# Kernel optimization log

Measured on AMD Instinct MI355X. Metric: run time of the kernel, lower is better.

The kernel has to match this reference:

```python
import jax, jax.numpy as jnp
import numpy as np

# Irrep layout of node_vec: 128x0e | 64x1e (64*3) | 32x2e (32*5)
MUL0, MUL1, MUL2 = 128, 64, 32
A = 32  # node_attr scalar channels (32x0e)
N = 8192


def setup_inputs() -> dict:
    key = jax.random.key(0)
    ks = jax.random.split(key, 12)
    f32 = jnp.float32
    return {
        "node_vec": jax.random.normal(ks[0], (N, MUL0 + 3 * MUL1 + 5 * MUL2), f32),
        "node_embedding": jax.random.normal(ks[1], (N, A), f32),
        # fctp_1: TP(input, attr) -> gated irreps (scalars + gates + vectors)
        "W1s": jax.random.normal(ks[2], (MUL0, A, MUL0), f32),          # 0e x 0e -> 0e
        "b1s": jnp.zeros((MUL0,), f32),
        "W1g": jax.random.normal(ks[3], (MUL0, A, MUL1 + MUL2), f32),   # 0e x 0e -> gate 0e
        "b1g": jnp.zeros((MUL1 + MUL2,), f32),
        "W1v1": jax.random.normal(ks[4], (MUL1, A, MUL1), f32),         # 1e x 0e -> 1e
        "W1v2": jax.random.normal(ks[5], (MUL2, A, MUL2), f32),         # 2e x 0e -> 2e
        # fctp_2: TP(mlp_mid, attr) -> 32x0e (only scalar path allowed by CG rules)
        "W2": jax.random.normal(ks[6], (MUL0, A, A), f32),
        "b2": jnp.zeros((A,), f32),
        # output network: LinearRS(32->32) + SiLU + LinearRS(32->1)
        "W3": jax.random.normal(ks[7], (A, A), f32),
        "b3": jnp.zeros((A,), f32),
        "W4": jax.random.normal(ks[8], (A, 1), f32),
        "b4": jnp.zeros((1,), f32),
    }


def reference(node_vec, node_embedding, W1s, b1s, W1g, b1g, W1v1, W1v2, W2, b2, W3, b3, W4, b4):
    n = node_vec.shape[0]
    attr = node_embedding
    # split features by irrep degree
    s = node_vec[:, :MUL0]                                         # [n,128]   0e
    v1 = node_vec[:, MUL0:MUL0 + 3 * MUL1].reshape(n, MUL1, 3)     # [n,64,3]  1e
    v2 = node_vec[:, MUL0 + 3 * MUL1:].reshape(n, MUL2, 5)         # [n,32,5]  2e

    inv = lambda u: 1.0 / np.sqrt(u * A).astype(np.float32)

    # ---- fctp_1: fully-connected TP with scalar attr (l x 0e -> l per-path mixing) ----
    s_mid = jnp.einsum('nu,nv,uvw->nw', s, attr, W1s) * inv(MUL0) + b1s
    g = jnp.einsum('nu,nv,uvw->nw', s, attr, W1g) * inv(MUL0) + b1g
    v1_mid = jnp.einsum('num,nv,uvw->nwm', v1, attr, W1v1) * inv(MUL1)
    v2_mid = jnp.einsum('num,nv,uvw->nwm', v2, attr, W1v2) * inv(MUL2)

    # ---- SwishGate: SiLU on scalars, sigmoid gates on vectors ----
    s_act = jax.nn.silu(s_mid)
    gate = jax.nn.sigmoid(g)
    v1_g = v1_mid * gate[:, :MUL1, None]
    v2_g = v2_mid * gate[:, MUL1:, None]
    # NOTE: v1_g/v2_g have no allowed CG path into the 0e output of fctp_2 (l x 0 -> 0
    # only for l=0), so they do not contribute — exactly as in the original module.
    del v1_g, v2_g

    # ---- fctp_2: mlp_mid x attr -> 32x0e (scalar path only) ----
    h = jnp.einsum('nu,nv,uvw->nw', s_act, attr, W2) * inv(MUL0) + b2

    # ---- output network: LinearRS + SiLU + LinearRS ----
    h = jax.nn.silu(h @ (W3 / np.sqrt(A).astype(np.float32)) + b3)
    pred_energy = h @ (W4 / np.sqrt(A).astype(np.float32)) + b4     # [n,1]
    return pred_energy
```

## Files before the change

kernel.cpp:

```cpp
#include <hip/hip_runtime.h>

typedef _Float16 f16;
typedef f16 f16x8 __attribute__((ext_vector_type(8)));
typedef f16 f16x4 __attribute__((ext_vector_type(4)));
typedef f16 f16x2 __attribute__((ext_vector_type(2)));
typedef float f32x4 __attribute__((ext_vector_type(4)));

union F8 { uint4 u4; f16x8 v; f16x2 h[4]; f16 e[8]; };

__global__ __launch_bounds__(256) void prep_kernel(
    const float* __restrict__ node_vec, const float* __restrict__ attr,
    const float* __restrict__ W1s, const float* __restrict__ W2,
    f16* __restrict__ s_f16, f16* __restrict__ attr_f16,
    f16* __restrict__ W1P, f16* __restrict__ W2P)
{
    __shared__ f16 T[32 * 36];
    const int b = blockIdx.x, t = threadIdx.x;

    if (b < 640) {
        const float* src; f16* dst; int u, w0, W;
        if (b < 512) { u = b >> 2; w0 = (b & 3) * 32; W = 128; src = W1s; dst = W1P; }
        else         { u = b - 512; w0 = 0;           W = 32;  src = W2;  dst = W2P; }
        {
            int v = t >> 3, wq = t & 7;
            float4 f = *(const float4*)(src + (size_t)(u * 32 + v) * W + w0 + wq * 4);
            T[v * 36 + wq * 4 + 0] = (f16)f.x;
            T[v * 36 + wq * 4 + 1] = (f16)f.y;
            T[v * 36 + wq * 4 + 2] = (f16)f.z;
            T[v * 36 + wq * 4 + 3] = (f16)f.w;
        }
        __syncthreads();
        {
            int w = t >> 3, vr = t & 7;
            f16x4 o = { T[(vr * 4 + 0) * 36 + w], T[(vr * 4 + 1) * 36 + w],
                        T[(vr * 4 + 2) * 36 + w], T[(vr * 4 + 3) * 36 + w] };
            *(f16x4*)(dst + (size_t)u * (W * 32) + (size_t)(w0 + w) * 32 + vr * 4) = o;
        }
    } else if (b < 1152) {
        int j = (b - 640) * 256 + t;
        int n = j >> 4, c = j & 15;
        float4 a  = *(const float4*)(node_vec + (size_t)n * 480 + c * 8);
        float4 bb = *(const float4*)(node_vec + (size_t)n * 480 + c * 8 + 4);
        f16x8 ev = { (f16)a.x, (f16)a.y, (f16)a.z, (f16)a.w,
                     (f16)bb.x, (f16)bb.y, (f16)bb.z, (f16)bb.w };
        *(f16x8*)(s_f16 + (size_t)n * 128 + c * 8) = ev;
    } else {
        int j = (b - 1152) * 256 + t;
        int n = j >> 2, c = j & 3;
        float4 a  = *(const float4*)(attr + (size_t)n * 32 + c * 8);
        float4 bb = *(const float4*)(attr + (size_t)n * 32 + c * 8 + 4);
        f16x8 ev = { (f16)a.x, (f16)a.y, (f16)a.z, (f16)a.w,
                     (f16)bb.x, (f16)bb.y, (f16)bb.z, (f16)bb.w };
        *(f16x8*)(attr_f16 + (size_t)n * 32 + c * 8) = ev;
    }
}

__global__ __launch_bounds__(256, 2) void gemm1_kernel(
    const f16* __restrict__ s_f16, const f16* __restrict__ attr_f16,
    const f16* __restrict__ W1P, const float* __restrict__ b1s,
    f16* __restrict__ s_act)
{
    __shared__ alignas(16) f16 s_lds[64 * 136];

    const int t  = threadIdx.x;
    const int n0 = blockIdx.x * 64;
    const int l  = t & 63, lr = l & 15, q = l >> 4;
    const int c0 = blockIdx.y * 64 + (t >> 6) * 16;

    const f16* Bp = W1P + ((size_t)(c0 + lr)) * 32 + q * 8;
    f16x8 B[8];
    #pragma unroll
    for (int j = 0; j < 8; ++j)
        B[j] = *(const f16x8*)(Bp + (size_t)j * 4096);

    F8 af[4];
    #pragma unroll
    for (int mt = 0; mt < 4; ++mt)
        af[mt].v = *(const f16x8*)(attr_f16 + (size_t)(n0 + 16 * mt + lr) * 32 + q * 8);

    #pragma unroll
    for (int i = 0; i < 4; ++i) {
        int ch = t + 256 * i;
        int r = ch >> 4, c8 = ch & 15;
        *(uint4*)(s_lds + r * 136 + c8 * 8) =
            *(const uint4*)(s_f16 + (size_t)(n0 + r) * 128 + c8 * 8);
    }
    __syncthreads();

    f32x4 acc[4] = { {0,0,0,0}, {0,0,0,0}, {0,0,0,0}, {0,0,0,0} };

    F8 s8[2][4];
    #pragma unroll
    for (int mt = 0; mt < 4; ++mt)
        s8[0][mt].v = *(const f16x8*)(s_lds + (16 * mt + lr) * 136);

    #pragma unroll 4
    for (int uo = 0; uo < 16; ++uo) {
        const int cur = uo & 1, nxt = cur ^ 1;
        const int uon = (uo + 1 < 16) ? uo + 1 : 15;
        #pragma unroll
        for (int mt = 0; mt < 4; ++mt)
            s8[nxt][mt].v = *(const f16x8*)(s_lds + (16 * mt + lr) * 136 + uon * 8);
        #pragma unroll
        for (int j = 0; j < 8; ++j) {
            const int u = uo * 8 + j;
            f16x8 bf = B[j];
            const int un = (u + 8 < 128) ? (u + 8) : u;
            B[j] = *(const f16x8*)(Bp + (size_t)un * 4096);
            #pragma unroll
            for (int mt = 0; mt < 4; ++mt) {
                f16 sv = s8[cur][mt].e[j];
                f16x2 sb = { sv, sv };
                F8 a;
                #pragma unroll
                for (int kk = 0; kk < 4; ++kk)
                    a.h[kk] = sb * af[mt].h[kk];
                acc[mt] = __builtin_amdgcn_mfma_f32_16x16x32_f16(a.v, bf, acc[mt], 0, 0, 0);
            }
        }
    }

    const float bv = b1s[c0 + lr];
    #pragma unroll
    for (int mt = 0; mt < 4; ++mt)
        #pragma unroll
        for (int reg = 0; reg < 4; ++reg) {
            int row = n0 + 16 * mt + q * 4 + reg;
            float v = acc[mt][reg] * 0.015625f + bv;
            s_act[(size_t)row * 128 + c0 + lr] = (f16)(v / (1.f + __expf(-v)));
        }
}

__global__ __launch_bounds__(256, 2) void gemm2_head_kernel(
    const f16* __restrict__ s_act, const f16* __restrict__ attr_f16,
    const f16* __restrict__ W2P, const float* __restrict__ b2,
    const float* __restrict__ W3, const float* __restrict__ b3,
    const float* __restrict__ W4, const float* __restrict__ b4,
    float* __restrict__ out)
{
    __shared__ alignas(16) f16 s_lds[32 * 136];
    __shared__ alignas(16) float red[4][32 * 36];
    __shared__ alignas(16) float W3_lds[32 * 36];
    __shared__ alignas(16) float h_lds[32 * 36];

    const int t  = threadIdx.x;
    const int n0 = blockIdx.x * 32;
    const int wv = t >> 6, l = t & 63, lr = l & 15, q = l >> 4;
    const int u0 = wv * 32;

    const f16* B2p = W2P + ((size_t)u0 * 32 + lr) * 32 + q * 8;
    f16x8 B0[8], B1[8];
    #pragma unroll
    for (int j = 0; j < 8; ++j) {
        B0[j] = *(const f16x8*)(B2p + (size_t)j * 1024);
        B1[j] = *(const f16x8*)(B2p + (size_t)j * 1024 + 512);
    }

    F8 af[2];
    #pragma unroll
    for (int mt = 0; mt < 2; ++mt)
        af[mt].v = *(const f16x8*)(attr_f16 + (size_t)(n0 + 16 * mt + lr) * 32 + q * 8);

    #pragma unroll
    for (int i = 0; i < 2; ++i) {
        int ch = t + 256 * i;
        int r = ch >> 4, c8 = ch & 15;
        *(uint4*)(s_lds + r * 136 + c8 * 8) =
            *(const uint4*)(s_act + (size_t)(n0 + r) * 128 + c8 * 8);
    }
    { int i = t >> 3, jj = (t & 7) * 4;
      *(f32x4*)(W3_lds + i * 36 + jj) = *(const f32x4*)(W3 + i * 32 + jj); }
    __syncthreads();

    f32x4 acc[2][2] = { { {0,0,0,0}, {0,0,0,0} }, { {0,0,0,0}, {0,0,0,0} } };

    F8 s8[2][2];
    #pragma unroll
    for (int mt = 0; mt < 2; ++mt)
        s8[0][mt].v = *(const f16x8*)(s_lds + (16 * mt + lr) * 136 + u0);

    #pragma unroll
    for (int uo = 0; uo < 4; ++uo) {
        const int cur = uo & 1, nxt = cur ^ 1;
        const int uon = (uo + 1 < 4) ? uo + 1 : 3;
        #pragma unroll
        for (int mt = 0; mt < 2; ++mt)
            s8[nxt][mt].v = *(const f16x8*)(s_lds + (16 * mt + lr) * 136 + u0 + uon * 8);
        #pragma unroll
        for (int j = 0; j < 8; ++j) {
            const int k = uo * 8 + j;
            f16x8 bf0 = B0[j], bf1 = B1[j];
            const int kn = (k + 8 < 32) ? (k + 8) : k;
            B0[j] = *(const f16x8*)(B2p + (size_t)kn * 1024);
            B1[j] = *(const f16x8*)(B2p + (size_t)kn * 1024 + 512);
            #pragma unroll
            for (int mt = 0; mt < 2; ++mt) {
                f16 sv = s8[cur][mt].e[j];
                f16x2 sb = { sv, sv };
                F8 a;
                #pragma unroll
                for (int kk = 0; kk < 4; ++kk)
                    a.h[kk] = sb * af[mt].h[kk];
                acc[mt][0] = __builtin_amdgcn_mfma_f32_16x16x32_f16(a.v, bf0, acc[mt][0], 0, 0, 0);
                acc[mt][1] = __builtin_amdgcn_mfma_f32_16x16x32_f16(a.v, bf1, acc[mt][1], 0, 0, 0);
            }
        }
    }

    #pragma unroll
    for (int mt = 0; mt < 2; ++mt)
        #pragma unroll
        for (int nt = 0; nt < 2; ++nt)
            #pragma unroll
            for (int reg = 0; reg < 4; ++reg)
                red[wv][(16 * mt + q * 4 + reg) * 36 + 16 * nt + lr] = acc[mt][nt][reg];
    __syncthreads();

    {
        int row = t >> 3, c4 = (t & 7) * 4;
        f32x4 s = *(const f32x4*)(&red[0][row * 36 + c4]);
        s = s + *(const f32x4*)(&red[1][row * 36 + c4]);
        s = s + *(const f32x4*)(&red[2][row * 36 + c4]);
        s = s + *(const f32x4*)(&red[3][row * 36 + c4]);
        #pragma unroll
        for (int e = 0; e < 4; ++e)
            h_lds[row * 36 + c4 + e] = s[e] * 0.015625f + b2[c4 + e];
    }
    __syncthreads();

    {
        int node = t >> 3, j4 = (t & 7) * 4;
        float a0 = 0.f, a1 = 0.f, a2 = 0.f, a3 = 0.f;
        #pragma unroll
        for (int i = 0; i < 32; ++i) {
            float hv = h_lds[node * 36 + i];
            a0 += hv * W3_lds[i * 36 + j4 + 0];
            a1 += hv * W3_lds[i * 36 + j4 + 1];
            a2 += hv * W3_lds[i * 36 + j4 + 2];
            a3 += hv * W3_lds[i * 36 + j4 + 3];
        }
        const float inv = 0.17677669529663687f;
        float p = 0.f;
        float aa[4] = { a0, a1, a2, a3 };
        #pragma unroll
        for (int e = 0; e < 4; ++e) {
            float tv = aa[e] * inv + b3[j4 + e];
            float g  = tv / (1.f + __expf(-tv));
            p += g * W4[j4 + e] * inv;
        }
        p += __shfl_xor(p, 1);
        p += __shfl_xor(p, 2);
        p += __shfl_xor(p, 4);
        if ((t & 7) == 0) out[n0 + node] = p + b4[0];
    }
}

extern "C" void kernel_launch(void* const* d_in, const int* in_sizes, int n_in,
                              void* d_out, int out_size, void* d_ws, size_t ws_size,
                              hipStream_t stream)
{
    const float* node_vec = (const float*)d_in[0];
    const float* attr     = (const float*)d_in[1];
    const float* W1s      = (const float*)d_in[2];
    const float* b1s      = (const float*)d_in[3];
    const float* W2       = (const float*)d_in[8];
    const float* b2       = (const float*)d_in[9];
    const float* W3       = (const float*)d_in[10];
    const float* b3       = (const float*)d_in[11];
    const float* W4       = (const float*)d_in[12];
    const float* b4       = (const float*)d_in[13];
    float* out = (float*)d_out;

    char* ws = (char*)d_ws;
    f16* s_f16    = (f16*)(ws);
    f16* attr_f16 = (f16*)(ws + (2u   << 20));
    f16* W1P      = (f16*)(ws + (2560u << 10));
    f16* W2P      = (f16*)(ws + (3584u << 10));
    f16* s_act    = (f16*)(ws + (3840u << 10));

    prep_kernel<<<1280, 256, 0, stream>>>(node_vec, attr, W1s, W2,
                                          s_f16, attr_f16, W1P, W2P);
    gemm1_kernel<<<dim3(128, 2), 256, 0, stream>>>(s_f16, attr_f16, W1P, b1s, s_act);
    gemm2_head_kernel<<<256, 256, 0, stream>>>(s_act, attr_f16, W2P, b2,
                                               W3, b3, W4, b4, out);
}
```

Before: 121.4 us.

## Fuse fp32-to-fp16 activation conversion into GEMM kernels and halve gemm1 row tile

Drops the separate prep passes that converted node_vec scalars and attr to fp16. gemm1 and gemm2 now read fp32 directly and convert while staging into LDS or registers, which removes a global round trip. gemm1's row tile shrinks from 64 to 32 nodes, doubling its grid to 512 blocks for better CU fill. The cost is less reuse of each B fragment per block, so weight traffic from L2 goes up, and gemm1 now issues strided fp32 loads.

```diff
diff --git a/kernel.cpp b/kernel.cpp
--- a/kernel.cpp
+++ b/kernel.cpp
@@ -9,130 +9,116 @@
 union F8 { uint4 u4; f16x8 v; f16x2 h[4]; f16 e[8]; };
 
 __global__ __launch_bounds__(256) void prep_kernel(
-    const float* __restrict__ node_vec, const float* __restrict__ attr,
     const float* __restrict__ W1s, const float* __restrict__ W2,
-    f16* __restrict__ s_f16, f16* __restrict__ attr_f16,
     f16* __restrict__ W1P, f16* __restrict__ W2P)
 {
     __shared__ f16 T[32 * 36];
     const int b = blockIdx.x, t = threadIdx.x;
 
-    if (b < 640) {
-        const float* src; f16* dst; int u, w0, W;
-        if (b < 512) { u = b >> 2; w0 = (b & 3) * 32; W = 128; src = W1s; dst = W1P; }
-        else         { u = b - 512; w0 = 0;           W = 32;  src = W2;  dst = W2P; }
-        {
-            int v = t >> 3, wq = t & 7;
-            float4 f = *(const float4*)(src + (size_t)(u * 32 + v) * W + w0 + wq * 4);
-            T[v * 36 + wq * 4 + 0] = (f16)f.x;
-            T[v * 36 + wq * 4 + 1] = (f16)f.y;
-            T[v * 36 + wq * 4 + 2] = (f16)f.z;
-            T[v * 36 + wq * 4 + 3] = (f16)f.w;
-        }
-        __syncthreads();
-        {
-            int w = t >> 3, vr = t & 7;
-            f16x4 o = { T[(vr * 4 + 0) * 36 + w], T[(vr * 4 + 1) * 36 + w],
-                        T[(vr * 4 + 2) * 36 + w], T[(vr * 4 + 3) * 36 + w] };
-            *(f16x4*)(dst + (size_t)u * (W * 32) + (size_t)(w0 + w) * 32 + vr * 4) = o;
-        }
-    } else if (b < 1152) {
-        int j = (b - 640) * 256 + t;
-        int n = j >> 4, c = j & 15;
-        float4 a  = *(const float4*)(node_vec + (size_t)n * 480 + c * 8);
-        float4 bb = *(const float4*)(node_vec + (size_t)n * 480 + c * 8 + 4);
-        f16x8 ev = { (f16)a.x, (f16)a.y, (f16)a.z, (f16)a.w,
-                     (f16)bb.x, (f16)bb.y, (f16)bb.z, (f16)bb.w };
-        *(f16x8*)(s_f16 + (size_t)n * 128 + c * 8) = ev;
-    } else {
-        int j = (b - 1152) * 256 + t;
-        int n = j >> 2, c = j & 3;
-        float4 a  = *(const float4*)(attr + (size_t)n * 32 + c * 8);
-        float4 bb = *(const float4*)(attr + (size_t)n * 32 + c * 8 + 4);
-        f16x8 ev = { (f16)a.x, (f16)a.y, (f16)a.z, (f16)a.w,
-                     (f16)bb.x, (f16)bb.y, (f16)bb.z, (f16)bb.w };
-        *(f16x8*)(attr_f16 + (size_t)n * 32 + c * 8) = ev;
+    const float* src; f16* dst; int u, w0, W;
+    if (b < 512) { u = b >> 2; w0 = (b & 3) * 32; W = 128; src = W1s; dst = W1P; }
+    else         { u = b - 512; w0 = 0;           W = 32;  src = W2;  dst = W2P; }
+    {
+        int v = t >> 3, wq = t & 7;
+        float4 f = *(const float4*)(src + (size_t)(u * 32 + v) * W + w0 + wq * 4);
+        T[v * 36 + wq * 4 + 0] = (f16)f.x;
+        T[v * 36 + wq * 4 + 1] = (f16)f.y;
+        T[v * 36 + wq * 4 + 2] = (f16)f.z;
+        T[v * 36 + wq * 4 + 3] = (f16)f.w;
+    }
+    __syncthreads();
+    {
+        int w = t >> 3, vr = t & 7;
+        f16x4 o = { T[(vr * 4 + 0) * 36 + w], T[(vr * 4 + 1) * 36 + w],
+                    T[(vr * 4 + 2) * 36 + w], T[(vr * 4 + 3) * 36 + w] };
+        *(f16x4*)(dst + (size_t)u * (W * 32) + (size_t)(w0 + w) * 32 + vr * 4) = o;
     }
 }
 
 __global__ __launch_bounds__(256, 2) void gemm1_kernel(
-    const f16* __restrict__ s_f16, const f16* __restrict__ attr_f16,
+    const float* __restrict__ node_vec, const float* __restrict__ attr,
     const f16* __restrict__ W1P, const float* __restrict__ b1s,
     f16* __restrict__ s_act)
 {
-    __shared__ alignas(16) f16 s_lds[64 * 136];
+    __shared__ alignas(16) f16 s_lds[32 * 136];
 
     const int t  = threadIdx.x;
-    const int n0 = blockIdx.x * 64;
+    const int n0 = blockIdx.x * 32;
     const int l  = t & 63, lr = l & 15, q = l >> 4;
     const int c0 = blockIdx.y * 64 + (t >> 6) * 16;
 
+    #pragma unroll
+    for (int i = 0; i < 4; ++i) {
+        int idx = t + 256 * i;
+        int r = idx >> 5, c4 = idx & 31;
+        float4 f = *(const float4*)(node_vec + (size_t)(n0 + r) * 480 + c4 * 4);
+        f16x4 o = { (f16)f.x, (f16)f.y, (f16)f.z, (f16)f.w };
+        *(f16x4*)(s_lds + r * 136 + c4 * 4) = o;
+    }
+
+    F8 af0, af1;
+    #pragma unroll
+    for (int kk = 0; kk < 4; ++kk) {
+        float2 fa = *(const float2*)(attr + (size_t)(n0 + lr) * 32 + q * 8 + kk * 2);
+        float2 fb = *(const float2*)(attr + (size_t)(n0 + 16 + lr) * 32 + q * 8 + kk * 2);
+        af0.h[kk] = f16x2{ (f16)fa.x, (f16)fa.y };
+        af1.h[kk] = f16x2{ (f16)fb.x, (f16)fb.y };
+    }
+
     const f16* Bp = W1P + ((size_t)(c0 + lr)) * 32 + q * 8;
     f16x8 B[8];
     #pragma unroll
     for (int j = 0; j < 8; ++j)
         B[j] = *(const f16x8*)(Bp + (size_t)j * 4096);
 
-    F8 af[4];
-    #pragma unroll
-    for (int mt = 0; mt < 4; ++mt)
-        af[mt].v = *(const f16x8*)(attr_f16 + (size_t)(n0 + 16 * mt + lr) * 32 + q * 8);
-
-    #pragma unroll
-    for (int i = 0; i < 4; ++i) {
-        int ch = t + 256 * i;
-        int r = ch >> 4, c8 = ch & 15;
-        *(uint4*)(s_lds + r * 136 + c8 * 8) =
-            *(const uint4*)(s_f16 + (size_t)(n0 + r) * 128 + c8 * 8);
-    }
-    __syncthreads();
-
-    f32x4 acc[4] = { {0,0,0,0}, {0,0,0,0}, {0,0,0,0}, {0,0,0,0} };
-
-    F8 s8[2][4];
-    #pragma unroll
-    for (int mt = 0; mt < 4; ++mt)
-        s8[0][mt].v = *(const f16x8*)(s_lds + (16 * mt + lr) * 136);
-
-    #pragma unroll 4
+    __syncthreads();
+
+    f32x4 acc0 = {0.f, 0.f, 0.f, 0.f}, acc1 = {0.f, 0.f, 0.f, 0.f};
+
+    F8 s8[2][2];
+    s8[0][0].v = *(const f16x8*)(s_lds + lr * 136);
+    s8[0][1].v = *(const f16x8*)(s_lds + (16 + lr) * 136);
+
+    #pragma unroll
     for (int uo = 0; uo < 16; ++uo) {
         const int cur = uo & 1, nxt = cur ^ 1;
         const int uon = (uo + 1 < 16) ? uo + 1 : 15;
-        #pragma unroll
-        for (int mt = 0; mt < 4; ++mt)
-            s8[nxt][mt].v = *(const f16x8*)(s_lds + (16 * mt + lr) * 136 + uon * 8);
+        s8[nxt][0].v = *(const f16x8*)(s_lds + lr * 136 + uon * 8);
+        s8[nxt][1].v = *(const f16x8*)(s_lds + (16 + lr) * 136 + uon * 8);
         #pragma unroll
         for (int j = 0; j < 8; ++j) {
             const int u = uo * 8 + j;
             f16x8 bf = B[j];
             const int un = (u + 8 < 128) ? (u + 8) : u;
             B[j] = *(const f16x8*)(Bp + (size_t)un * 4096);
+            f16 sv0 = s8[cur][0].e[j];
+            f16 sv1 = s8[cur][1].e[j];
+            f16x2 sb0 = { sv0, sv0 }, sb1 = { sv1, sv1 };
+            F8 a0, a1;
             #pragma unroll
-            for (int mt = 0; mt < 4; ++mt) {
-                f16 sv = s8[cur][mt].e[j];
-                f16x2 sb = { sv, sv };
-                F8 a;
-                #pragma unroll
-                for (int kk = 0; kk < 4; ++kk)
-                    a.h[kk] = sb * af[mt].h[kk];
-                acc[mt] = __builtin_amdgcn_mfma_f32_16x16x32_f16(a.v, bf, acc[mt], 0, 0, 0);
+            for (int kk = 0; kk < 4; ++kk) {
+                a0.h[kk] = sb0 * af0.h[kk];
+                a1.h[kk] = sb1 * af1.h[kk];
             }
+            acc0 = __builtin_amdgcn_mfma_f32_16x16x32_f16(a0.v, bf, acc0, 0, 0, 0);
+            acc1 = __builtin_amdgcn_mfma_f32_16x16x32_f16(a1.v, bf, acc1, 0, 0, 0);
         }
     }
 
     const float bv = b1s[c0 + lr];
     #pragma unroll
-    for (int mt = 0; mt < 4; ++mt)
-        #pragma unroll
-        for (int reg = 0; reg < 4; ++reg) {
-            int row = n0 + 16 * mt + q * 4 + reg;
-            float v = acc[mt][reg] * 0.015625f + bv;
-            s_act[(size_t)row * 128 + c0 + lr] = (f16)(v / (1.f + __expf(-v)));
-        }
+    for (int reg = 0; reg < 4; ++reg) {
+        float v0 = acc0[reg] * 0.015625f + bv;
+        float v1 = acc1[reg] * 0.015625f + bv;
+        s_act[(size_t)(n0 + q * 4 + reg) * 128 + c0 + lr] =
+            (f16)(v0 / (1.f + __expf(-v0)));
+        s_act[(size_t)(n0 + 16 + q * 4 + reg) * 128 + c0 + lr] =
+            (f16)(v1 / (1.f + __expf(-v1)));
+    }
 }
 
 __global__ __launch_bounds__(256, 2) void gemm2_head_kernel(
-    const f16* __restrict__ s_act, const f16* __restrict__ attr_f16,
+    const f16* __restrict__ s_act, const float* __restrict__ attr,
     const f16* __restrict__ W2P, const float* __restrict__ b2,
     const float* __restrict__ W3, const float* __restrict__ b3,
     const float* __restrict__ W4, const float* __restrict__ b4,
@@ -156,10 +142,14 @@
         B1[j] = *(const f16x8*)(B2p + (size_t)j * 1024 + 512);
     }
 
-    F8 af[2];
-    #pragma unroll
-    for (int mt = 0; mt < 2; ++mt)
-        af[mt].v = *(const f16x8*)(attr_f16 + (size_t)(n0 + 16 * mt + lr) * 32 + q * 8);
+    F8 af0, af1;
+    #pragma unroll
+    for (int kk = 0; kk < 4; ++kk) {
+        float2 fa = *(const float2*)(attr + (size_t)(n0 + lr) * 32 + q * 8 + kk * 2);
+        float2 fb = *(const float2*)(attr + (size_t)(n0 + 16 + lr) * 32 + q * 8 + kk * 2);
+        af0.h[kk] = f16x2{ (f16)fa.x, (f16)fa.y };
+        af1.h[kk] = f16x2{ (f16)fb.x, (f16)fb.y };
+    }
 
     #pragma unroll
     for (int i = 0; i < 2; ++i) {
@@ -172,20 +162,19 @@
       *(f32x4*)(W3_lds + i * 36 + jj) = *(const f32x4*)(W3 + i * 32 + jj); }
     __syncthreads();
 
-    f32x4 acc[2][2] = { { {0,0,0,0}, {0,0,0,0} }, { {0,0,0,0}, {0,0,0,0} } };
+    f32x4 acc00 = {0,0,0,0}, acc01 = {0,0,0,0};
+    f32x4 acc10 = {0,0,0,0}, acc11 = {0,0,0,0};
 
     F8 s8[2][2];
-    #pragma unroll
-    for (int mt = 0; mt < 2; ++mt)
-        s8[0][mt].v = *(const f16x8*)(s_lds + (16 * mt + lr) * 136 + u0);
+    s8[0][0].v = *(const f16x8*)(s_lds + lr * 136 + u0);
+    s8[0][1].v = *(const f16x8*)(s_lds + (16 + lr) * 136 + u0);
 
     #pragma unroll
     for (int uo = 0; uo < 4; ++uo) {
         const int cur = uo & 1, nxt = cur ^ 1;
         const int uon = (uo + 1 < 4) ? uo + 1 : 3;
-        #pragma unroll
-        for (int mt = 0; mt < 2; ++mt)
-            s8[nxt][mt].v = *(const f16x8*)(s_lds + (16 * mt + lr) * 136 + u0 + uon * 8);
+        s8[nxt][0].v = *(const f16x8*)(s_lds + lr * 136 + u0 + uon * 8);
+        s8[nxt][1].v = *(const f16x8*)(s_lds + (16 + lr) * 136 + u0 + uon * 8);
         #pragma unroll
         for (int j = 0; j < 8; ++j) {
             const int k = uo * 8 + j;
@@ -193,27 +182,29 @@
             const int kn = (k + 8 < 32) ? (k + 8) : k;
             B0[j] = *(const f16x8*)(B2p + (size_t)kn * 1024);
             B1[j] = *(const f16x8*)(B2p + (size_t)kn * 1024 + 512);
+            f16 sv0 = s8[cur][0].e[j];
+            f16 sv1 = s8[cur][1].e[j];
+            f16x2 sb0 = { sv0, sv0 }, sb1 = { sv1, sv1 };
+            F8 a0, a1;
             #pragma unroll
-            for (int mt = 0; mt < 2; ++mt) {
-                f16 sv = s8[cur][mt].e[j];
-                f16x2 sb = { sv, sv };
-                F8 a;
-                #pragma unroll
-                for (int kk = 0; kk < 4; ++kk)
-                    a.h[kk] = sb * af[mt].h[kk];
-                acc[mt][0] = __builtin_amdgcn_mfma_f32_16x16x32_f16(a.v, bf0, acc[mt][0], 0, 0, 0);
-                acc[mt][1] = __builtin_amdgcn_mfma_f32_16x16x32_f16(a.v, bf1, acc[mt][1], 0, 0, 0);
+            for (int kk = 0; kk < 4; ++kk) {
+                a0.h[kk] = sb0 * af0.h[kk];
+                a1.h[kk] = sb1 * af1.h[kk];
             }
-        }
-    }
-
-    #pragma unroll
-    for (int mt = 0; mt < 2; ++mt)
-        #pragma unroll
-        for (int nt = 0; nt < 2; ++nt)
-            #pragma unroll
-            for (int reg = 0; reg < 4; ++reg)
-                red[wv][(16 * mt + q * 4 + reg) * 36 + 16 * nt + lr] = acc[mt][nt][reg];
+            acc00 = __builtin_amdgcn_mfma_f32_16x16x32_f16(a0.v, bf0, acc00, 0, 0, 0);
+            acc01 = __builtin_amdgcn_mfma_f32_16x16x32_f16(a0.v, bf1, acc01, 0, 0, 0);
+            acc10 = __builtin_amdgcn_mfma_f32_16x16x32_f16(a1.v, bf0, acc10, 0, 0, 0);
+            acc11 = __builtin_amdgcn_mfma_f32_16x16x32_f16(a1.v, bf1, acc11, 0, 0, 0);
+        }
+    }
+
+    #pragma unroll
+    for (int reg = 0; reg < 4; ++reg) {
+        red[wv][(q * 4 + reg) * 36 + lr]           = acc00[reg];
+        red[wv][(q * 4 + reg) * 36 + 16 + lr]      = acc01[reg];
+        red[wv][(16 + q * 4 + reg) * 36 + lr]      = acc10[reg];
+        red[wv][(16 + q * 4 + reg) * 36 + 16 + lr] = acc11[reg];
+    }
     __syncthreads();
 
     {
@@ -272,15 +263,12 @@
     float* out = (float*)d_out;
 
     char* ws = (char*)d_ws;
-    f16* s_f16    = (f16*)(ws);
-    f16* attr_f16 = (f16*)(ws + (2u   << 20));
-    f16* W1P      = (f16*)(ws + (2560u << 10));
-    f16* W2P      = (f16*)(ws + (3584u << 10));
-    f16* s_act    = (f16*)(ws + (3840u << 10));
-
-    prep_kernel<<<1280, 256, 0, stream>>>(node_vec, attr, W1s, W2,
-                                          s_f16, attr_f16, W1P, W2P);
-    gemm1_kernel<<<dim3(128, 2), 256, 0, stream>>>(s_f16, attr_f16, W1P, b1s, s_act);
-    gemm2_head_kernel<<<256, 256, 0, stream>>>(s_act, attr_f16, W2P, b2,
+    f16* W1P   = (f16*)(ws);
+    f16* W2P   = (f16*)(ws + (1u << 20));
+    f16* s_act = (f16*)(ws + (1280u << 10));
+
+    prep_kernel<<<640, 256, 0, stream>>>(W1s, W2, W1P, W2P);
+    gemm1_kernel<<<dim3(256, 2), 256, 0, stream>>>(node_vec, attr, W1P, b1s, s_act);
+    gemm2_head_kernel<<<256, 256, 0, stream>>>(s_act, attr, W2P, b2,
                                                W3, b3, W4, b4, out);
 }
```

Result: faster. 117.0 us (-3.6%).
